# Kernel tuning notes

Measured on AMD Instinct MI355X. Metric: run time of the kernel, lower is better.

The kernel has to match this reference:

```python
import jax, jax.numpy as jnp
import numpy as np

B, N, C, H, W, NH, SR = 16, 4096, 128, 64, 64, 4, 8
LN_EPS = 1e-5


def _conv(x, w, b, stride, padding, groups=1):
    y = jax.lax.conv_general_dilated(
        x, w, (stride, stride), padding,
        feature_group_count=groups,
        dimension_numbers=('NCHW', 'OIHW', 'NCHW'))
    return y + b[None, :, None, None]


def _layernorm(x, g, b):
    m = jnp.mean(x, axis=-1, keepdims=True)
    v = jnp.mean((x - m) ** 2, axis=-1, keepdims=True)
    return (x - m) / jnp.sqrt(v + LN_EPS) * g + b


def setup_inputs() -> dict:
    key = jax.random.key(0)
    ks = jax.random.split(key, 12)
    s = 0.02
    return {
        'x': jax.random.normal(ks[0], (B, N, C), jnp.float32),
        'q_w': jax.random.normal(ks[1], (C, C), jnp.float32) * s,
        'sr1_w': jax.random.normal(ks[2], (C, C, SR, SR), jnp.float32) * s,
        'sr1_b': jnp.zeros((C,), jnp.float32),
        'n1_g': jnp.ones((C,), jnp.float32),
        'n1_b': jnp.zeros((C,), jnp.float32),
        'sr2_w': jax.random.normal(ks[3], (C, C, SR // 2, SR // 2), jnp.float32) * s,
        'sr2_b': jnp.zeros((C,), jnp.float32),
        'n2_g': jnp.ones((C,), jnp.float32),
        'n2_b': jnp.zeros((C,), jnp.float32),
        'kv1_w': jax.random.normal(ks[4], (C, C), jnp.float32) * s,
        'kv2_w': jax.random.normal(ks[5], (C, C), jnp.float32) * s,
        'lc1_w': jax.random.normal(ks[6], (C // 2, 1, 3, 3), jnp.float32) * s,
        'lc1_b': jnp.zeros((C // 2,), jnp.float32),
        'lc2_w': jax.random.normal(ks[7], (C // 2, 1, 3, 3), jnp.float32) * s,
        'lc2_b': jnp.zeros((C // 2,), jnp.float32),
        'proj_w': jax.random.normal(ks[8], (C, C), jnp.float32) * s,
        'proj_b': jnp.zeros((C,), jnp.float32),
        'h': H,
        'w': W,
    }


def _forward(x, q_w, sr1_w, sr1_b, n1_g, n1_b, sr2_w, sr2_b, n2_g, n2_b,
             kv1_w, kv2_w, lc1_w, lc1_b, lc2_w, lc2_b, proj_w, proj_b, h, w):
    b, n, c = x.shape
    nh, sr = NH, SR
    hh = nh // 2          # heads per branch
    d = c // nh           # head dim
    scale = d ** -0.5

    q = (x @ q_w.T).reshape(b, n, nh, d).transpose(0, 2, 1, 3)  # (b,nh,n,d)
    x_img = x.transpose(0, 2, 1).reshape(b, c, h, w)

    def branch(sr_w, sr_b, g, beta, kv_w, lc_w, lc_b, stride, q_part):
        hp, wp = h // stride, w // stride
        m = hp * wp
        t = _conv(x_img, sr_w, sr_b, stride, 'VALID')          # (b,c,hp,wp)
        t = t.reshape(b, c, m).transpose(0, 2, 1)              # (b,m,c)
        t = jax.nn.gelu(_layernorm(t, g, beta), approximate=False)
        kv = (t @ kv_w.T).reshape(b, m, 2, hh, d).transpose(2, 0, 3, 1, 4)
        k, v = kv[0], kv[1]                                    # (b,hh,m,d)
        attn = jax.nn.softmax(
            jnp.einsum('bhnd,bhmd->bhnm', q_part, k) * scale, axis=-1)
        # local depthwise conv on v over the reduced spatial grid
        v_img = v.transpose(0, 2, 1, 3).reshape(b, m, c // 2)
        v_img = v_img.transpose(0, 2, 1).reshape(b, c // 2, hp, wp)
        v_loc = _conv(v_img, lc_w, lc_b, 1, [(1, 1), (1, 1)], groups=c // 2)
        v = v + v_loc.reshape(b, hh, d, m).transpose(0, 1, 3, 2)
        out = jnp.einsum('bhnm,bhmd->bhnd', attn, v)           # (b,hh,n,d)
        return out.transpose(0, 2, 1, 3).reshape(b, n, c // 2)

    x1 = branch(sr1_w, sr1_b, n1_g, n1_b, kv1_w, lc1_w, lc1_b, sr, q[:, :hh])
    x2 = branch(sr2_w, sr2_b, n2_g, n2_b, kv2_w, lc2_w, lc2_b, sr // 2, q[:, hh:])
    return jnp.concatenate([x1, x2], axis=-1) @ proj_w.T + proj_b


def reference(x, q_w, sr1_w, sr1_b, n1_g, n1_b, sr2_w, sr2_b, n2_g, n2_b,
              kv1_w, kv2_w, lc1_w, lc1_b, lc2_w, lc2_b, proj_w, proj_b, h, w):
    return _forward(x, q_w, sr1_w, sr1_b, n1_g, n1_b, sr2_w, sr2_b, n2_g, n2_b,
                    kv1_w, kv2_w, lc1_w, lc1_b, lc2_w, lc2_b, proj_w, proj_b, h, w)
```

## Files before the change

### kernel.cpp

```cpp
#include <hip/hip_runtime.h>
#include <math.h>

#define B_ 16
#define N_ 4096

typedef __attribute__((ext_vector_type(8))) short short8v;
typedef __attribute__((ext_vector_type(4))) short short4v;
typedef __attribute__((ext_vector_type(4))) float f32x4;

__device__ __forceinline__ unsigned short f2bf(float f) {
  unsigned int u = __float_as_uint(f);
  return (unsigned short)((u + 0x7FFFu + ((u >> 16) & 1u)) >> 16);
}

__device__ __forceinline__ unsigned int pk2(float a, float b) {
  return (unsigned int)f2bf(a) | ((unsigned int)f2bf(b) << 16);
}

__device__ __forceinline__ short8v cvt8f(const float* p) {
  float4 a = *reinterpret_cast<const float4*>(p);
  float4 b = *reinterpret_cast<const float4*>(p + 4);
  short8v r;
  r[0] = (short)f2bf(a.x); r[1] = (short)f2bf(a.y);
  r[2] = (short)f2bf(a.z); r[3] = (short)f2bf(a.w);
  r[4] = (short)f2bf(b.x); r[5] = (short)f2bf(b.y);
  r[6] = (short)f2bf(b.z); r[7] = (short)f2bf(b.w);
  return r;
}

__global__ __launch_bounds__(256) void prep(const float* __restrict__ x,
    unsigned short* __restrict__ xT, const float* __restrict__ a,
    const float* __restrict__ b, const float* __restrict__ c,
    const float* __restrict__ d, const float* __restrict__ s1,
    const float* __restrict__ s2, unsigned short* __restrict__ wa,
    unsigned short* __restrict__ wb, unsigned short* __restrict__ wc,
    unsigned short* __restrict__ wd, unsigned short* __restrict__ w1,
    unsigned short* __restrict__ w2) {
  __shared__ float lds[32 * 132];
  const int t = threadIdx.x;
  if (blockIdx.x < 2048) {
    const int bb = blockIdx.x >> 7, pt = blockIdx.x & 127;
    const int ptile = pt * 32;
    for (int i = t; i < 1024; i += 256) {
      int p = i >> 5, c4 = (i & 31) << 2;
      *reinterpret_cast<float4*>(&lds[p * 132 + c4]) =
          *reinterpret_cast<const float4*>(
              x + ((size_t)(bb * 4096 + ptile + p)) * 128 + c4);
    }
    __syncthreads();
    const int ch = t >> 1, p0 = (t & 1) * 16;
    unsigned short* dst = xT + (size_t)bb * 524288 + ch * 4096 + ptile + p0;
    uint4 u0, u1;
    u0.x = pk2(lds[(p0 + 0) * 132 + ch], lds[(p0 + 1) * 132 + ch]);
    u0.y = pk2(lds[(p0 + 2) * 132 + ch], lds[(p0 + 3) * 132 + ch]);
    u0.z = pk2(lds[(p0 + 4) * 132 + ch], lds[(p0 + 5) * 132 + ch]);
    u0.w = pk2(lds[(p0 + 6) * 132 + ch], lds[(p0 + 7) * 132 + ch]);
    u1.x = pk2(lds[(p0 + 8) * 132 + ch], lds[(p0 + 9) * 132 + ch]);
    u1.y = pk2(lds[(p0 + 10) * 132 + ch], lds[(p0 + 11) * 132 + ch]);
    u1.z = pk2(lds[(p0 + 12) * 132 + ch], lds[(p0 + 13) * 132 + ch]);
    u1.w = pk2(lds[(p0 + 14) * 132 + ch], lds[(p0 + 15) * 132 + ch]);
    *reinterpret_cast<uint4*>(dst) = u0;
    *reinterpret_cast<uint4*>(dst + 8) = u1;
  } else {
    int i = (blockIdx.x - 2048) * 256 + t;
    if (i < 16384) wa[i] = f2bf(a[i]);
    else if (i < 32768) { int o = i - 16384; wb[o] = f2bf(b[o]); }
    else if (i < 49152) { int o = i - 32768; wc[o] = f2bf(c[o]); }
    else if (i < 65536) { int o = i - 49152; wd[o] = f2bf(d[o]); }
    else if (i < 65536 + 1048576) { int o = i - 65536; w1[o] = f2bf(s1[o]); }
    else { int o = i - 65536 - 1048576; w2[o] = f2bf(s2[o]); }
  }
}

template <int SRV, int KSP>
__device__ void conv_body(int bx, int by, const unsigned short* __restrict__ xT,
    const unsigned short* __restrict__ W, float* __restrict__ part) {
  constexpr int WP = 64 / SRV;
  constexpr int M = WP * WP;
  constexpr int ROWS = B_ * M;
  constexpr int SS = SRV * SRV;
  constexpr int KTOT = 128 * SS;
  constexpr int LSS = (SRV == 8) ? 6 : 4;
  constexpr int LM = (SRV == 8) ? 6 : 8;
  constexpr int LWP = (SRV == 8) ? 3 : 4;
  const int t = threadIdx.x;
  const int wid = t >> 6, lane = t & 63;
  const int lrow = lane & 15, lk = (lane >> 4) << 3;
  const int r0 = bx * 128 + wid * 32;
  const int kb0 = by * KSP;
  int rbase[2], pixoff[2];
#pragma unroll
  for (int m = 0; m < 2; m++) {
    int row = r0 + m * 16 + lrow;
    int b = row >> LM, p = row & (M - 1);
    int ph = p >> LWP, pw = p & (WP - 1);
    rbase[m] = b << 19;
    pixoff[m] = (ph * SRV) * 64 + pw * SRV;
  }
  f32x4 acc[2][8];
#pragma unroll
  for (int m = 0; m < 2; m++)
#pragma unroll
    for (int n = 0; n < 8; n++) acc[m][n] = (f32x4)(0.f);
  for (int k0 = 0; k0 < KSP; k0 += 32) {
    int k = kb0 + k0 + lk;
    int ci = k >> LSS;
    int rem = k & (SS - 1);
    short8v a[2], bf[8];
#pragma unroll
    for (int m = 0; m < 2; m++) {
      if constexpr (SRV == 8) {
        a[m] = *reinterpret_cast<const short8v*>(
            xT + (size_t)rbase[m] + ci * 4096 + pixoff[m] + (rem >> 3) * 64);
      } else {
        int kh0 = rem >> 2;
        short4v lo = *reinterpret_cast<const short4v*>(
            xT + (size_t)rbase[m] + ci * 4096 + pixoff[m] + kh0 * 64);
        short4v hi = *reinterpret_cast<const short4v*>(
            xT + (size_t)rbase[m] + ci * 4096 + pixoff[m] + (kh0 + 1) * 64);
        short8v av;
        av[0] = lo[0]; av[1] = lo[1]; av[2] = lo[2]; av[3] = lo[3];
        av[4] = hi[0]; av[5] = hi[1]; av[6] = hi[2]; av[7] = hi[3];
        a[m] = av;
      }
    }
#pragma unroll
    for (int n = 0; n < 8; n++)
      bf[n] = *reinterpret_cast<const short8v*>(
          W + (size_t)(n * 16 + lrow) * KTOT + k);
#pragma unroll
    for (int m = 0; m < 2; m++)
#pragma unroll
      for (int n = 0; n < 8; n++)
        acc[m][n] = __builtin_amdgcn_mfma_f32_16x16x32_bf16(a[m], bf[n],
                                                            acc[m][n], 0, 0, 0);
  }
  const int rr = (lane >> 4) << 2;
#pragma unroll
  for (int m = 0; m < 2; m++)
#pragma unroll
    for (int n = 0; n < 8; n++) {
      int cc = n * 16 + lrow;
#pragma unroll
      for (int j = 0; j < 4; j++)
        part[((size_t)by * ROWS + r0 + m * 16 + rr + j) * 128 + cc] =
            acc[m][n][j];
    }
}

template <bool A_BF16, bool OUT_BF16, bool HAS_BIAS>
__device__ void gemm_body(int bx, const void* __restrict__ Araw,
    const unsigned short* __restrict__ W, const float* __restrict__ bias,
    void* __restrict__ out) {
  const int t = threadIdx.x;
  const int wid = t >> 6, lane = t & 63;
  const int lrow = lane & 15, lk = (lane >> 4) << 3;
  const int r0 = bx * 128 + wid * 32;
  f32x4 acc[2][8];
#pragma unroll
  for (int m = 0; m < 2; m++)
#pragma unroll
    for (int n = 0; n < 8; n++) acc[m][n] = (f32x4)(0.f);
#pragma unroll
  for (int k0 = 0; k0 < 128; k0 += 32) {
    short8v a[2], bf[8];
#pragma unroll
    for (int m = 0; m < 2; m++) {
      if constexpr (A_BF16)
        a[m] = *reinterpret_cast<const short8v*>(
            (const unsigned short*)Araw + (size_t)(r0 + m * 16 + lrow) * 128 +
            k0 + lk);
      else
        a[m] = cvt8f((const float*)Araw + (size_t)(r0 + m * 16 + lrow) * 128 +
                     k0 + lk);
    }
#pragma unroll
    for (int n = 0; n < 8; n++)
      bf[n] = *reinterpret_cast<const short8v*>(
          W + (size_t)(n * 16 + lrow) * 128 + k0 + lk);
#pragma unroll
    for (int m = 0; m < 2; m++)
#pragma unroll
      for (int n = 0; n < 8; n++)
        acc[m][n] = __builtin_amdgcn_mfma_f32_16x16x32_bf16(a[m], bf[n],
                                                            acc[m][n], 0, 0, 0);
  }
  const int rr = (lane >> 4) << 2;
#pragma unroll
  for (int m = 0; m < 2; m++)
#pragma unroll
    for (int n = 0; n < 8; n++) {
      int cc = n * 16 + lrow;
      float bv = HAS_BIAS ? bias[cc] : 0.f;
#pragma unroll
      for (int j = 0; j < 4; j++) {
        size_t idx = (size_t)(r0 + m * 16 + rr + j) * 128 + cc;
        float v = acc[m][n][j] + bv;
        if constexpr (OUT_BF16)
          ((unsigned short*)out)[idx] = f2bf(v);
        else
          ((float*)out)[idx] = v;
      }
    }
}

__global__ __launch_bounds__(256) void conv_q(
    const unsigned short* __restrict__ xT, const unsigned short* __restrict__ w1b,
    const unsigned short* __restrict__ w2b, float* __restrict__ part1,
    float* __restrict__ part2, const float* __restrict__ x,
    const unsigned short* __restrict__ wq, unsigned short* __restrict__ qb) {
  const int bid = blockIdx.x;
  if (bid < 256) {
    conv_body<8, 256>(bid & 7, bid >> 3, xT, w1b, part1);
  } else if (bid < 512) {
    int j = bid - 256;
    conv_body<4, 256>(j & 31, j >> 5, xT, w2b, part2);
  } else {
    gemm_body<false, true, false>(bid - 512, x, wq, nullptr, qb);
  }
}

__global__ __launch_bounds__(128) void ln_all(const float* __restrict__ part1,
    const float* __restrict__ part2, const float* __restrict__ cb1,
    const float* __restrict__ g1, const float* __restrict__ be1,
    const float* __restrict__ cb2, const float* __restrict__ g2,
    const float* __restrict__ be2, unsigned short* __restrict__ out1,
    unsigned short* __restrict__ out2) {
  const int t = threadIdx.x;
  int row = blockIdx.x;
  const float* part; const float *cb, *g, *be; unsigned short* out;
  int nsplit, rows;
  if (row < 1024) {
    part = part1; cb = cb1; g = g1; be = be1; out = out1;
    nsplit = 32; rows = 1024;
  } else {
    row -= 1024;
    part = part2; cb = cb2; g = g2; be = be2; out = out2;
    nsplit = 8; rows = 4096;
  }
  float v = cb[t];
  for (int s = 0; s < nsplit; s++)
    v += part[((size_t)s * rows + row) * 128 + t];
  float sv = v, sq = v * v;
#pragma unroll
  for (int off = 32; off > 0; off >>= 1) {
    sv += __shfl_down(sv, off, 64);
    sq += __shfl_down(sq, off, 64);
  }
  __shared__ float red0[2], red1[2];
  if ((t & 63) == 0) {
    red0[t >> 6] = sv;
    red1[t >> 6] = sq;
  }
  __syncthreads();
  float mean = (red0[0] + red0[1]) * (1.f / 128.f);
  float var = (red1[0] + red1[1]) * (1.f / 128.f) - mean * mean;
  float y = (v - mean) * rsqrtf(var + 1e-5f) * g[t] + be[t];
  out[(size_t)row * 128 + t] = f2bf(y * 0.5f * (1.f + erff(y * 0.70710678118f)));
}

__device__ void kv_body(int bx, const unsigned short* __restrict__ A,
    const unsigned short* __restrict__ W, unsigned short* __restrict__ kb,
    float* __restrict__ vr) {
  const int t = threadIdx.x;
  const int wid = t >> 6, lane = t & 63;
  const int lrow = lane & 15, lk = (lane >> 4) << 3;
  const int r0 = bx * 128 + wid * 32;
  f32x4 acc[2][8];
#pragma unroll
  for (int m = 0; m < 2; m++)
#pragma unroll
    for (int n = 0; n < 8; n++) acc[m][n] = (f32x4)(0.f);
#pragma unroll
  for (int k0 = 0; k0 < 128; k0 += 32) {
    short8v a[2], bf[8];
#pragma unroll
    for (int m = 0; m < 2; m++)
      a[m] = *reinterpret_cast<const short8v*>(
          A + (size_t)(r0 + m * 16 + lrow) * 128 + k0 + lk);
#pragma unroll
    for (int n = 0; n < 8; n++)
      bf[n] = *reinterpret_cast<const short8v*>(
          W + (size_t)(n * 16 + lrow) * 128 + k0 + lk);
#pragma unroll
    for (int m = 0; m < 2; m++)
#pragma unroll
      for (int n = 0; n < 8; n++)
        acc[m][n] = __builtin_amdgcn_mfma_f32_16x16x32_bf16(a[m], bf[n],
                                                            acc[m][n], 0, 0, 0);
  }
  const int rr = (lane >> 4) << 2;
#pragma unroll
  for (int m = 0; m < 2; m++)
#pragma unroll
    for (int n = 0; n < 8; n++) {
      int cc = n * 16 + lrow;
#pragma unroll
      for (int j = 0; j < 4; j++) {
        int r = r0 + m * 16 + rr + j;
        float v = acc[m][n][j];
        if (cc < 64)
          kb[(size_t)r * 64 + cc] = f2bf(v);
        else
          vr[(size_t)r * 64 + (cc - 64)] = v;
      }
    }
}

__global__ __launch_bounds__(256) void kv_all(
    const unsigned short* __restrict__ t1b, const unsigned short* __restrict__ wkv1,
    unsigned short* __restrict__ kb1, float* __restrict__ vr1,
    const unsigned short* __restrict__ t2b, const unsigned short* __restrict__ wkv2,
    unsigned short* __restrict__ kb2, float* __restrict__ vr2) {
  if (blockIdx.x < 8)
    kv_body(blockIdx.x, t1b, wkv1, kb1, vr1);
  else
    kv_body(blockIdx.x - 8, t2b, wkv2, kb2, vr2);
}

template <int WP>
__device__ void dw_body(int idx, const float* __restrict__ vr,
    const float* __restrict__ lw, const float* __restrict__ lb,
    float* __restrict__ vp) {
  constexpr int M = WP * WP;
  constexpr int LM = (WP == 8) ? 6 : 8;
  constexpr int LWPc = (WP == 8) ? 3 : 4;
  int ch = idx & 63;
  int rest = idx >> 6;
  int m = rest & (M - 1);
  int bb = rest >> LM;
  int y = m >> LWPc, x0 = m & (WP - 1);
  float s = lb[ch];
#pragma unroll
  for (int ky = 0; ky < 3; ky++) {
    int yy = y + ky - 1;
    if (yy < 0 || yy >= WP) continue;
#pragma unroll
    for (int kx = 0; kx < 3; kx++) {
      int xx = x0 + kx - 1;
      if (xx < 0 || xx >= WP) continue;
      s += vr[((size_t)(bb * M + yy * WP + xx)) * 64 + ch] *
           lw[ch * 9 + ky * 3 + kx];
    }
  }
  vp[idx] = vr[((size_t)(bb * M + m)) * 64 + ch] + s;
}

__global__ __launch_bounds__(256) void dw_all(const float* __restrict__ vr1,
    const float* __restrict__ lw1, const float* __restrict__ lb1,
    float* __restrict__ v1p, const float* __restrict__ vr2,
    const float* __restrict__ lw2, const float* __restrict__ lb2,
    float* __restrict__ v2p) {
  if (blockIdx.x < 256)
    dw_body<8>(blockIdx.x * 256 + threadIdx.x, vr1, lw1, lb1, v1p);
  else
    dw_body<16>((blockIdx.x - 256) * 256 + threadIdx.x, vr2, lw2, lb2, v2p);
}

template <int M>
__device__ void tv_body(int blk, const float* __restrict__ vp,
    unsigned short* __restrict__ vT, float* lds) {
  constexpr int TPB = M / 32;
  const int t = threadIdx.x;
  const int b = blk / TPB, mt = blk % TPB;
  const int m0 = mt * 32;
  for (int i = t; i < 512; i += 256) {
    int m = i >> 4, c4 = (i & 15) << 2;
    *reinterpret_cast<float4*>(&lds[m * 68 + c4]) =
        *reinterpret_cast<const float4*>(vp + ((size_t)(b * M + m0 + m)) * 64 + c4);
  }
  __syncthreads();
  const int c = t >> 2, ms = (t & 3) * 8;
  unsigned short* dst = vT + ((size_t)b * 64 + c) * M + m0 + ms;
  uint4 u;
  u.x = pk2(lds[(ms + 0) * 68 + c], lds[(ms + 1) * 68 + c]);
  u.y = pk2(lds[(ms + 2) * 68 + c], lds[(ms + 3) * 68 + c]);
  u.z = pk2(lds[(ms + 4) * 68 + c], lds[(ms + 5) * 68 + c]);
  u.w = pk2(lds[(ms + 6) * 68 + c], lds[(ms + 7) * 68 + c]);
  *reinterpret_cast<uint4*>(dst) = u;
}

__global__ __launch_bounds__(256) void tv_all(const float* __restrict__ v1p,
    unsigned short* __restrict__ vT1, const float* __restrict__ v2p,
    unsigned short* __restrict__ vT2) {
  __shared__ float lds[32 * 68];
  if (blockIdx.x < 32)
    tv_body<64>(blockIdx.x, v1p, vT1, lds);
  else
    tv_body<256>(blockIdx.x - 32, v2p, vT2, lds);
}

template <int M, int QOFF>
__device__ void attn_body(int bx, int b, const unsigned short* __restrict__ qb,
    const unsigned short* __restrict__ kb, const unsigned short* __restrict__ vT,
    unsigned short* __restrict__ xc, unsigned short* Pl) {
  constexpr int HM = (M > 128) ? 128 : M;
  constexpr int NCH = M / HM;
  constexpr int PSTR = HM + 8;
  constexpr int MT = M / 16;
  constexpr int HKS = HM / 32;
  const int t = threadIdx.x;
  const int wid = t >> 6, lane = t & 63;
  const int lrow = lane & 15, g = lane >> 4;
  const int lk = g * 8;
  unsigned short* Plw = Pl + wid * 16 * PSTR;
  const size_t bm = (size_t)b * M;
  const int q0 = bx * 64 + wid * 16;
  const size_t qrow = ((size_t)b * 4096 + q0 + lrow) * 128;
  const float scale = 0.17677669529663687f;
#pragma unroll
  for (int h = 0; h < 2; h++) {
    const int qoff = QOFF + h * 32;
    short8v qf = *reinterpret_cast<const short8v*>(qb + qrow + qoff + lk);
    f32x4 s[MT];
#pragma unroll
    for (int mt = 0; mt < MT; mt++) {
      short8v kf = *reinterpret_cast<const short8v*>(
          kb + (bm + mt * 16 + lrow) * 64 + h * 32 + lk);
      s[mt] =
          __builtin_amdgcn_mfma_f32_16x16x32_bf16(kf, qf, (f32x4)(0.f), 0, 0, 0);
    }
    float l = 0.f;
#pragma unroll
    for (int mt = 0; mt < MT; mt++)
#pragma unroll
      for (int j = 0; j < 4; j++) {
        float p = __expf(s[mt][j] * scale);
        s[mt][j] = p;
        l += p;
      }
    l += __shfl_xor(l, 16, 64);
    l += __shfl_xor(l, 32, 64);
    f32x4 o[2];
    o[0] = (f32x4)(0.f);
    o[1] = (f32x4)(0.f);
#pragma unroll
    for (int half = 0; half < NCH; half++) {
#pragma unroll
      for (int mt2 = 0; mt2 < HM / 16; mt2++) {
        int mt = half * (HM / 16) + mt2;
        uint2 pw;
        pw.x = pk2(s[mt][0], s[mt][1]);
        pw.y = pk2(s[mt][2], s[mt][3]);
        *reinterpret_cast<uint2*>(&Plw[lrow * PSTR + mt2 * 16 + 4 * g]) = pw;
      }
      f32x4 oh[2];
      oh[0] = (f32x4)(0.f);
      oh[1] = (f32x4)(0.f);
#pragma unroll
      for (int ks = 0; ks < HKS; ks++) {
        short8v pf = *reinterpret_cast<const short8v*>(
            &Plw[lrow * PSTR + ks * 32 + lk]);
#pragma unroll
        for (int dt = 0; dt < 2; dt++) {
          short8v vf = *reinterpret_cast<const short8v*>(
              vT + ((size_t)b * 64 + h * 32 + dt * 16 + lrow) * M +
              half * HM + ks * 32 + lk);
          oh[dt] = __builtin_amdgcn_mfma_f32_16x16x32_bf16(vf, pf, oh[dt],
                                                           0, 0, 0);
        }
      }
#pragma unroll
      for (int dt = 0; dt < 2; dt++) o[dt] += oh[dt];
    }
    float linv = 1.f / l;
    unsigned short* orow = xc + qrow + qoff;
#pragma unroll
    for (int dt = 0; dt < 2; dt++) {
      uint2 u;
      u.x = pk2(o[dt][0] * linv, o[dt][1] * linv);
      u.y = pk2(o[dt][2] * linv, o[dt][3] * linv);
      *reinterpret_cast<uint2*>(orow + dt * 16 + 4 * g) = u;
    }
  }
}

__global__ __launch_bounds__(256) void attn_all(
    const unsigned short* __restrict__ qb, const unsigned short* __restrict__ kb1,
    const unsigned short* __restrict__ vT1, const unsigned short* __restrict__ kb2,
    const unsigned short* __restrict__ vT2, unsigned short* __restrict__ xc) {
  __shared__ unsigned short Pl[4 * 16 * 136];
  const int bid = blockIdx.x;
  if (bid < 1024)
    attn_body<256, 64>(bid & 63, bid >> 6, qb, kb2, vT2, xc, Pl);
  else {
    int j = bid - 1024;
    attn_body<64, 0>(j & 63, j >> 6, qb, kb1, vT1, xc, Pl);
  }
}

__global__ __launch_bounds__(256) void proj(const unsigned short* __restrict__ A,
    const unsigned short* __restrict__ W, const float* __restrict__ bias,
    float* __restrict__ out) {
  gemm_body<true, false, true>(blockIdx.x, A, W, bias, out);
}

extern "C" void kernel_launch(void* const* d_in, const int* in_sizes, int n_in,
                              void* d_out, int out_size, void* d_ws,
                              size_t ws_size, hipStream_t stream) {
  (void)in_sizes; (void)n_in; (void)out_size; (void)ws_size;
  const float* x      = (const float*)d_in[0];
  const float* q_w    = (const float*)d_in[1];
  const float* sr1_w  = (const float*)d_in[2];
  const float* sr1_b  = (const float*)d_in[3];
  const float* n1_g   = (const float*)d_in[4];
  const float* n1_b   = (const float*)d_in[5];
  const float* sr2_w  = (const float*)d_in[6];
  const float* sr2_b  = (const float*)d_in[7];
  const float* n2_g   = (const float*)d_in[8];
  const float* n2_b   = (const float*)d_in[9];
  const float* kv1_w  = (const float*)d_in[10];
  const float* kv2_w  = (const float*)d_in[11];
  const float* lc1_w  = (const float*)d_in[12];
  const float* lc1_b  = (const float*)d_in[13];
  const float* lc2_w  = (const float*)d_in[14];
  const float* lc2_b  = (const float*)d_in[15];
  const float* proj_w = (const float*)d_in[16];
  const float* proj_b = (const float*)d_in[17];

  char* w = (char*)d_ws;
  unsigned short* wq    = (unsigned short*)(w);
  unsigned short* wkv1  = (unsigned short*)(w + 32768);
  unsigned short* wkv2  = (unsigned short*)(w + 65536);
  unsigned short* wproj = (unsigned short*)(w + 98304);
  unsigned short* w1b   = (unsigned short*)(w + 131072);
  unsigned short* w2b   = (unsigned short*)(w + 2228224);
  unsigned short* xT  = (unsigned short*)(w + 2752512);
  unsigned short* qb  = (unsigned short*)(w + 2752512);
  unsigned short* kb1 = (unsigned short*)(w + 19529728);
  unsigned short* kb2 = (unsigned short*)(w + 19660800);
  float* part1 = (float*)(w + 33685504);
  float* part2 = (float*)(w + 33685504 + 16777216);
  unsigned short* xcb = (unsigned short*)(w + 33685504);
  unsigned short* t1b = (unsigned short*)(w + 69468160);
  unsigned short* t2b = (unsigned short*)(w + 69730304);
  float* vr1 = (float*)(w + 70778880);
  float* vr2 = (float*)(w + 71041024);
  float* v1p = (float*)(w + 72089600);
  float* v2p = (float*)(w + 72351744);
  unsigned short* vT1 = (unsigned short*)(w + 73400320);
  unsigned short* vT2 = (unsigned short*)(w + 73531392);

  prep<<<7424, 256, 0, stream>>>(x, xT, q_w, kv1_w, kv2_w, proj_w, sr1_w, sr2_w,
                                 wq, wkv1, wkv2, wproj, w1b, w2b);
  conv_q<<<1024, 256, 0, stream>>>(xT, w1b, w2b, part1, part2, x, wq, qb);
  ln_all<<<5120, 128, 0, stream>>>(part1, part2, sr1_b, n1_g, n1_b, sr2_b, n2_g,
                                   n2_b, t1b, t2b);
  kv_all<<<40, 256, 0, stream>>>(t1b, wkv1, kb1, vr1, t2b, wkv2, kb2, vr2);
  dw_all<<<1280, 256, 0, stream>>>(vr1, lc1_w, lc1_b, v1p, vr2, lc2_w, lc2_b, v2p);
  tv_all<<<160, 256, 0, stream>>>(v1p, vT1, v2p, vT2);
  attn_all<<<2048, 256, 0, stream>>>(qb, kb1, vT1, kb2, vT2, xcb);
  proj<<<512, 256, 0, stream>>>(xcb, wproj, proj_b, (float*)d_out);
}
```

Before: 133.7 us.

## Stage K tiles in LDS and merge both attention branches per block

The attention kernel now has each block handle one batch and query tile for both branches. At the start it copies that batch's K for the stride-4 and stride-8 branches into padded shared-memory arrays, then reads K fragments from LDS instead of global memory. This halves the grid to 1024 blocks and cuts repeated global K loads across the four waves. In exchange, LDS use per block rises to about 50 KB, which can lower occupancy, and each block does more serial work after a barrier.

```diff
diff --git a/kernel.cpp b/kernel.cpp
--- a/kernel.cpp
+++ b/kernel.cpp
@@ -391,87 +391,81 @@
 }
 
 template <int M, int QOFF>
-__device__ void attn_body(int bx, int b, const unsigned short* __restrict__ qb,
-    const unsigned short* __restrict__ kb, const unsigned short* __restrict__ vT,
-    unsigned short* __restrict__ xc, unsigned short* Pl) {
+__device__ void attn_head(int b, int q0, int h,
+    const unsigned short* __restrict__ qb, const unsigned short* Ks,
+    const unsigned short* __restrict__ vT, unsigned short* __restrict__ xc,
+    unsigned short* Plw) {
   constexpr int HM = (M > 128) ? 128 : M;
   constexpr int NCH = M / HM;
   constexpr int PSTR = HM + 8;
   constexpr int MT = M / 16;
   constexpr int HKS = HM / 32;
-  const int t = threadIdx.x;
-  const int wid = t >> 6, lane = t & 63;
+  const int lane = threadIdx.x & 63;
   const int lrow = lane & 15, g = lane >> 4;
   const int lk = g * 8;
-  unsigned short* Plw = Pl + wid * 16 * PSTR;
-  const size_t bm = (size_t)b * M;
-  const int q0 = bx * 64 + wid * 16;
   const size_t qrow = ((size_t)b * 4096 + q0 + lrow) * 128;
+  const int qoff = QOFF + h * 32;
   const float scale = 0.17677669529663687f;
-#pragma unroll
-  for (int h = 0; h < 2; h++) {
-    const int qoff = QOFF + h * 32;
-    short8v qf = *reinterpret_cast<const short8v*>(qb + qrow + qoff + lk);
-    f32x4 s[MT];
-#pragma unroll
-    for (int mt = 0; mt < MT; mt++) {
-      short8v kf = *reinterpret_cast<const short8v*>(
-          kb + (bm + mt * 16 + lrow) * 64 + h * 32 + lk);
-      s[mt] =
-          __builtin_amdgcn_mfma_f32_16x16x32_bf16(kf, qf, (f32x4)(0.f), 0, 0, 0);
-    }
-    float l = 0.f;
-#pragma unroll
-    for (int mt = 0; mt < MT; mt++)
-#pragma unroll
-      for (int j = 0; j < 4; j++) {
-        float p = __expf(s[mt][j] * scale);
-        s[mt][j] = p;
-        l += p;
+  short8v qf = *reinterpret_cast<const short8v*>(qb + qrow + qoff + lk);
+  f32x4 s[MT];
+#pragma unroll
+  for (int mt = 0; mt < MT; mt++) {
+    short8v kf = *reinterpret_cast<const short8v*>(
+        Ks + (mt * 16 + lrow) * 72 + h * 32 + lk);
+    s[mt] =
+        __builtin_amdgcn_mfma_f32_16x16x32_bf16(kf, qf, (f32x4)(0.f), 0, 0, 0);
+  }
+  float l = 0.f;
+#pragma unroll
+  for (int mt = 0; mt < MT; mt++)
+#pragma unroll
+    for (int j = 0; j < 4; j++) {
+      float p = __expf(s[mt][j] * scale);
+      s[mt][j] = p;
+      l += p;
+    }
+  l += __shfl_xor(l, 16, 64);
+  l += __shfl_xor(l, 32, 64);
+  f32x4 o[2];
+  o[0] = (f32x4)(0.f);
+  o[1] = (f32x4)(0.f);
+#pragma unroll
+  for (int half = 0; half < NCH; half++) {
+#pragma unroll
+    for (int mt2 = 0; mt2 < HM / 16; mt2++) {
+      int mt = half * (HM / 16) + mt2;
+      uint2 pw;
+      pw.x = pk2(s[mt][0], s[mt][1]);
+      pw.y = pk2(s[mt][2], s[mt][3]);
+      *reinterpret_cast<uint2*>(&Plw[lrow * PSTR + mt2 * 16 + 4 * g]) = pw;
+    }
+    f32x4 oh[2];
+    oh[0] = (f32x4)(0.f);
+    oh[1] = (f32x4)(0.f);
+#pragma unroll
+    for (int ks = 0; ks < HKS; ks++) {
+      short8v pf = *reinterpret_cast<const short8v*>(
+          &Plw[lrow * PSTR + ks * 32 + lk]);
+#pragma unroll
+      for (int dt = 0; dt < 2; dt++) {
+        short8v vf = *reinterpret_cast<const short8v*>(
+            vT + ((size_t)b * 64 + h * 32 + dt * 16 + lrow) * M + half * HM +
+            ks * 32 + lk);
+        oh[dt] =
+            __builtin_amdgcn_mfma_f32_16x16x32_bf16(vf, pf, oh[dt], 0, 0, 0);
       }
-    l += __shfl_xor(l, 16, 64);
-    l += __shfl_xor(l, 32, 64);
-    f32x4 o[2];
-    o[0] = (f32x4)(0.f);
-    o[1] = (f32x4)(0.f);
-#pragma unroll
-    for (int half = 0; half < NCH; half++) {
-#pragma unroll
-      for (int mt2 = 0; mt2 < HM / 16; mt2++) {
-        int mt = half * (HM / 16) + mt2;
-        uint2 pw;
-        pw.x = pk2(s[mt][0], s[mt][1]);
-        pw.y = pk2(s[mt][2], s[mt][3]);
-        *reinterpret_cast<uint2*>(&Plw[lrow * PSTR + mt2 * 16 + 4 * g]) = pw;
-      }
-      f32x4 oh[2];
-      oh[0] = (f32x4)(0.f);
-      oh[1] = (f32x4)(0.f);
-#pragma unroll
-      for (int ks = 0; ks < HKS; ks++) {
-        short8v pf = *reinterpret_cast<const short8v*>(
-            &Plw[lrow * PSTR + ks * 32 + lk]);
-#pragma unroll
-        for (int dt = 0; dt < 2; dt++) {
-          short8v vf = *reinterpret_cast<const short8v*>(
-              vT + ((size_t)b * 64 + h * 32 + dt * 16 + lrow) * M +
-              half * HM + ks * 32 + lk);
-          oh[dt] = __builtin_amdgcn_mfma_f32_16x16x32_bf16(vf, pf, oh[dt],
-                                                           0, 0, 0);
-        }
-      }
-#pragma unroll
-      for (int dt = 0; dt < 2; dt++) o[dt] += oh[dt];
-    }
-    float linv = 1.f / l;
-    unsigned short* orow = xc + qrow + qoff;
-#pragma unroll
-    for (int dt = 0; dt < 2; dt++) {
-      uint2 u;
-      u.x = pk2(o[dt][0] * linv, o[dt][1] * linv);
-      u.y = pk2(o[dt][2] * linv, o[dt][3] * linv);
-      *reinterpret_cast<uint2*>(orow + dt * 16 + 4 * g) = u;
-    }
+    }
+#pragma unroll
+    for (int dt = 0; dt < 2; dt++) o[dt] += oh[dt];
+  }
+  float linv = 1.f / l;
+  unsigned short* orow = xc + qrow + qoff;
+#pragma unroll
+  for (int dt = 0; dt < 2; dt++) {
+    uint2 u;
+    u.x = pk2(o[dt][0] * linv, o[dt][1] * linv);
+    u.y = pk2(o[dt][2] * linv, o[dt][3] * linv);
+    *reinterpret_cast<uint2*>(orow + dt * 16 + 4 * g) = u;
   }
 }
 
@@ -479,14 +473,31 @@
     const unsigned short* __restrict__ qb, const unsigned short* __restrict__ kb1,
     const unsigned short* __restrict__ vT1, const unsigned short* __restrict__ kb2,
     const unsigned short* __restrict__ vT2, unsigned short* __restrict__ xc) {
+  __shared__ unsigned short Ks2[256 * 72];
+  __shared__ unsigned short Ks1[64 * 72];
   __shared__ unsigned short Pl[4 * 16 * 136];
-  const int bid = blockIdx.x;
-  if (bid < 1024)
-    attn_body<256, 64>(bid & 63, bid >> 6, qb, kb2, vT2, xc, Pl);
-  else {
-    int j = bid - 1024;
-    attn_body<64, 0>(j & 63, j >> 6, qb, kb1, vT1, xc, Pl);
-  }
+  const int t = threadIdx.x;
+  const int b = blockIdx.x >> 6, qt = blockIdx.x & 63;
+  for (int i = t; i < 2048; i += 256) {
+    int row = i >> 3, seg = i & 7;
+    *reinterpret_cast<uint4*>(&Ks2[row * 72 + seg * 8]) =
+        *reinterpret_cast<const uint4*>(kb2 + ((size_t)b * 256 + row) * 64 +
+                                        seg * 8);
+  }
+  for (int i = t; i < 512; i += 256) {
+    int row = i >> 3, seg = i & 7;
+    *reinterpret_cast<uint4*>(&Ks1[row * 72 + seg * 8]) =
+        *reinterpret_cast<const uint4*>(kb1 + ((size_t)b * 64 + row) * 64 +
+                                        seg * 8);
+  }
+  __syncthreads();
+  const int wid = t >> 6;
+  unsigned short* Plw = Pl + wid * 16 * 136;
+  const int q0 = qt * 64 + wid * 16;
+  attn_head<256, 64>(b, q0, 0, qb, Ks2, vT2, xc, Plw);
+  attn_head<256, 64>(b, q0, 1, qb, Ks2, vT2, xc, Plw);
+  attn_head<64, 0>(b, q0, 0, qb, Ks1, vT1, xc, Plw);
+  attn_head<64, 0>(b, q0, 1, qb, Ks1, vT1, xc, Plw);
 }
 
 __global__ __launch_bounds__(256) void proj(const unsigned short* __restrict__ A,
@@ -549,6 +560,6 @@
   kv_all<<<40, 256, 0, stream>>>(t1b, wkv1, kb1, vr1, t2b, wkv2, kb2, vr2);
   dw_all<<<1280, 256, 0, stream>>>(vr1, lc1_w, lc1_b, v1p, vr2, lc2_w, lc2_b, v2p);
   tv_all<<<160, 256, 0, stream>>>(v1p, vT1, v2p, vT2);
-  attn_all<<<2048, 256, 0, stream>>>(qb, kb1, vT1, kb2, vT2, xcb);
+  attn_all<<<1024, 256, 0, stream>>>(qb, kb1, vT1, kb2, vT2, xcb);
   proj<<<512, 256, 0, stream>>>(xcb, wproj, proj_b, (float*)d_out);
 }
```

Result: faster. 124.2 us (-7.1%).
